# Kernel tuning notes

Hardware: AMD Instinct MI355X
Metric: run time of the kernel (lower is better)

Reference implementation:

```python
import jax, jax.numpy as jnp
import numpy as np

N_NODES = 100000
N_EDGES = 800000
HIDDEN = 128


def setup_inputs() -> dict:
    key = jax.random.key(0)
    k1, k2, k3, k4, k5, k6 = jax.random.split(key, 6)
    z = jax.random.normal(k1, (N_NODES, HIDDEN), dtype=jnp.float32)
    edge_index = jax.random.randint(k2, (2, N_EDGES), 0, N_NODES, dtype=jnp.int64)
    # nn.Linear params (torch default init scale ~ 1/sqrt(fan_in))
    s1 = 1.0 / np.sqrt(2 * HIDDEN)
    s2 = 1.0 / np.sqrt(HIDDEN)
    W1 = jax.random.uniform(k3, (2 * HIDDEN, HIDDEN), jnp.float32, -s1, s1)
    b1 = jax.random.uniform(k4, (HIDDEN,), jnp.float32, -s1, s1)
    W2 = jax.random.uniform(k5, (HIDDEN, 1), jnp.float32, -s2, s2)
    b2 = jax.random.uniform(k6, (1,), jnp.float32, -s2, s2)
    return {"z": z, "edge_index": edge_index, "W1": W1, "b1": b1, "W2": W2, "b2": b2}


def reference(z, edge_index, W1, b1, W2, b2):
    src, dst = edge_index[0], edge_index[1]
    # Gather endpoint features: [E, H] each. Avoid materializing the [E, 2H]
    # concat by splitting W1 into src/dst halves (same math as cat + matmul).
    W1_src, W1_dst = W1[:HIDDEN], W1[HIDDEN:]
    h = z[src] @ W1_src + z[dst] @ W1_dst + b1  # [E, H]
    h = jax.nn.relu(h)
    score = h @ W2 + b2  # [E, 1]
    return score
```

## Files before the change

### kernel.cpp

```cpp
#include <hip/hip_runtime.h>
#include <hip/hip_bf16.h>

#define N_NODES 100000
#define N_EDGES 800000
#define HIDDEN 128
#define N_TILES 1563
#define PC_GRID 512

typedef short frag_ab __attribute__((ext_vector_type(8)));
typedef float frag_cd __attribute__((ext_vector_type(4)));

__device__ inline unsigned short f2b(float f) {
    union { float f; unsigned u; } x; x.f = f;
    return (unsigned short)((x.u + 0x7fffu + ((x.u >> 16) & 1u)) >> 16);
}

__device__ inline unsigned pk2(float x, float y) {
    union { __hip_bfloat162 h; unsigned u; } c;
    c.h = __float22bfloat162_rn(make_float2(x, y));
    return c.u;
}

__global__ __launch_bounds__(256) void transpose_w1(
    const float* __restrict__ W1, unsigned short* __restrict__ Bt)
{
    const int t  = threadIdx.x;
    const int nc = blockIdx.x * 4 + (t >> 6);
    const int k2 = (t & 63) * 2;
    const int col  = nc & 127;
    const int roff = (nc >= 128) ? 128 : 0;
    float f0 = W1[(size_t)(roff + k2)     * HIDDEN + col];
    float f1 = W1[(size_t)(roff + k2 + 1) * HIDDEN + col];
    *(unsigned*)(Bt + (size_t)nc * HIDDEN + k2) = (unsigned)f2b(f0) | ((unsigned)f2b(f1) << 16);
}

#define AS_STRIDE 136
#define CS_STRIDE 264

__global__ __launch_bounds__(256) void precompute_uv_mfma(
    const float* __restrict__ z, const unsigned short* __restrict__ Bt,
    const float* __restrict__ b1, unsigned short* __restrict__ UV)
{
    __shared__ unsigned short smem[64 * CS_STRIDE];
    const int t = threadIdx.x;
    const int lane = t & 63;
    const int w = t >> 6;
    const int wn = w * 64;
    const int g  = lane >> 4;
    const int lc = lane & 15;

    frag_ab b[4][4];
    float bias[4];
    #pragma unroll
    for (int nt = 0; nt < 4; ++nt) {
        int nc = wn + nt * 16 + lc;
        bias[nt] = (nc < HIDDEN) ? b1[nc] : 0.f;
        const unsigned short* brow = Bt + (size_t)nc * HIDDEN;
        #pragma unroll
        for (int q = 0; q < 4; ++q)
            b[nt][q] = *(const frag_ab*)(brow + q * 32 + g * 8);
    }

    int tile = blockIdx.x;
    uint2 pf[8];
    #pragma unroll
    for (int i = 0; i < 8; ++i) {
        int f4 = i * 256 + t;
        int m = tile * 64 + (f4 >> 5);
        if (m >= N_NODES) m = N_NODES - 1;
        float4 v = ((const float4*)z)[(size_t)m * 32 + (f4 & 31)];
        pf[i].x = pk2(v.x, v.y);
        pf[i].y = pk2(v.z, v.w);
    }

    while (true) {
        #pragma unroll
        for (int i = 0; i < 8; ++i) {
            int f4 = i * 256 + t;
            *(uint2*)&smem[(f4 >> 5) * AS_STRIDE + (f4 & 31) * 4] = pf[i];
        }
        __syncthreads();

        const int next = tile + PC_GRID;
        const bool have_next = (next < N_TILES);
        if (have_next) {
            #pragma unroll
            for (int i = 0; i < 8; ++i) {
                int f4 = i * 256 + t;
                int m = next * 64 + (f4 >> 5);
                if (m >= N_NODES) m = N_NODES - 1;
                float4 v = ((const float4*)z)[(size_t)m * 32 + (f4 & 31)];
                pf[i].x = pk2(v.x, v.y);
                pf[i].y = pk2(v.z, v.w);
            }
        }

        frag_cd acc[4][4];
        #pragma unroll
        for (int mt = 0; mt < 4; ++mt)
            #pragma unroll
            for (int nt = 0; nt < 4; ++nt)
                acc[mt][nt] = (frag_cd){0.f, 0.f, 0.f, 0.f};
        #pragma unroll
        for (int q = 0; q < 4; ++q) {
            frag_ab a[4];
            #pragma unroll
            for (int mt = 0; mt < 4; ++mt)
                a[mt] = *(const frag_ab*)&smem[(mt * 16 + lc) * AS_STRIDE + q * 32 + g * 8];
            #pragma unroll
            for (int mt = 0; mt < 4; ++mt)
                #pragma unroll
                for (int nt = 0; nt < 4; ++nt)
                    acc[mt][nt] = __builtin_amdgcn_mfma_f32_16x16x32_bf16(
                        a[mt], b[nt][q], acc[mt][nt], 0, 0, 0);
        }
        __syncthreads();

        #pragma unroll
        for (int nt = 0; nt < 4; ++nt) {
            int nc = wn + nt * 16 + lc;
            #pragma unroll
            for (int mt = 0; mt < 4; ++mt)
                #pragma unroll
                for (int r = 0; r < 4; ++r)
                    smem[(mt * 16 + g * 4 + r) * CS_STRIDE + nc] =
                        f2b(acc[mt][nt][r] + bias[nt]);
        }
        __syncthreads();

        const int m0 = tile * 64;
        #pragma unroll
        for (int i = 0; i < 8; ++i) {
            int f = i * 256 + t;
            int m = f >> 5;
            int c16 = f & 31;
            if (m0 + m < N_NODES) {
                uint4 val = *(const uint4*)&smem[m * CS_STRIDE + c16 * 8];
                *(uint4*)&UV[(size_t)(m0 + m) * 256 + c16 * 8] = val;
            }
        }
        if (!have_next) break;
        __syncthreads();
        tile = next;
    }
}

__device__ inline float2 bf2(unsigned u) {
    union { unsigned i; float f; } lo, hi;
    lo.i = u << 16;
    hi.i = u & 0xffff0000u;
    return make_float2(lo.f, hi.f);
}

__device__ inline float2 rfma2(unsigned u, unsigned v, float2 w, float2 acc) {
    float2 uf = bf2(u), vf = bf2(v);
    float2 s = make_float2(uf.x + vf.x, uf.y + vf.y);
    s.x = fmaxf(s.x, 0.f); s.y = fmaxf(s.y, 0.f);
    acc.x = __builtin_fmaf(s.x, w.x, acc.x);
    acc.y = __builtin_fmaf(s.y, w.y, acc.y);
    return acc;
}

__global__ __launch_bounds__(256) void edge_score(
    const int* __restrict__ ei, const unsigned short* __restrict__ UV,
    const float* __restrict__ W2, const float* __restrict__ B2,
    float* __restrict__ out)
{
    const int t = threadIdx.x;
    const int g = t & 7;
    const int slot = t >> 3;
    const int e0 = blockIdx.x * 64 + slot;
    const int e1 = e0 + 32;

    const float4* W24 = (const float4*)W2;
    const float4 w0 = W24[g * 4 + 0];
    const float4 w1 = W24[g * 4 + 1];
    const float4 w2 = W24[g * 4 + 2];
    const float4 w3 = W24[g * 4 + 3];

    const int s0 = ei[e0];
    const int d0 = ei[N_EDGES + e0];
    const int s1 = ei[e1];
    const int d1 = ei[N_EDGES + e1];

    const uint4* u0p = (const uint4*)(UV + (size_t)s0 * 256) + g * 2;
    const uint4* v0p = (const uint4*)(UV + (size_t)d0 * 256 + 128) + g * 2;
    const uint4* u1p = (const uint4*)(UV + (size_t)s1 * 256) + g * 2;
    const uint4* v1p = (const uint4*)(UV + (size_t)d1 * 256 + 128) + g * 2;
    const uint4 ua0 = u0p[0], ub0 = u0p[1];
    const uint4 va0 = v0p[0], vb0 = v0p[1];
    const uint4 ua1 = u1p[0], ub1 = u1p[1];
    const uint4 va1 = v1p[0], vb1 = v1p[1];

    float2 A = make_float2(0.f, 0.f), B = make_float2(0.f, 0.f);
    A = rfma2(ua0.x, va0.x, make_float2(w0.x, w0.y), A);
    A = rfma2(ua0.y, va0.y, make_float2(w0.z, w0.w), A);
    A = rfma2(ua0.z, va0.z, make_float2(w1.x, w1.y), A);
    A = rfma2(ua0.w, va0.w, make_float2(w1.z, w1.w), A);
    A = rfma2(ub0.x, vb0.x, make_float2(w2.x, w2.y), A);
    A = rfma2(ub0.y, vb0.y, make_float2(w2.z, w2.w), A);
    A = rfma2(ub0.z, vb0.z, make_float2(w3.x, w3.y), A);
    A = rfma2(ub0.w, vb0.w, make_float2(w3.z, w3.w), A);

    B = rfma2(ua1.x, va1.x, make_float2(w0.x, w0.y), B);
    B = rfma2(ua1.y, va1.y, make_float2(w0.z, w0.w), B);
    B = rfma2(ua1.z, va1.z, make_float2(w1.x, w1.y), B);
    B = rfma2(ua1.w, va1.w, make_float2(w1.z, w1.w), B);
    B = rfma2(ub1.x, vb1.x, make_float2(w2.x, w2.y), B);
    B = rfma2(ub1.y, vb1.y, make_float2(w2.z, w2.w), B);
    B = rfma2(ub1.z, vb1.z, make_float2(w3.x, w3.y), B);
    B = rfma2(ub1.w, vb1.w, make_float2(w3.z, w3.w), B);

    float sa = A.x + A.y;
    float sb = B.x + B.y;
    sa += __shfl_xor(sa, 1, 8);
    sa += __shfl_xor(sa, 2, 8);
    sa += __shfl_xor(sa, 4, 8);
    sb += __shfl_xor(sb, 1, 8);
    sb += __shfl_xor(sb, 2, 8);
    sb += __shfl_xor(sb, 4, 8);

    if (g == 0) {
        float bb = B2[0];
        out[e0] = sa + bb;
        out[e1] = sb + bb;
    }
}

extern "C" void kernel_launch(void* const* d_in, const int* in_sizes, int n_in,
                              void* d_out, int out_size, void* d_ws, size_t ws_size,
                              hipStream_t stream) {
    const float* z  = (const float*)d_in[0];
    const int*   ei = (const int*)d_in[1];
    const float* W1 = (const float*)d_in[2];
    const float* b1 = (const float*)d_in[3];
    const float* W2 = (const float*)d_in[4];
    const float* b2 = (const float*)d_in[5];
    float* out = (float*)d_out;

    unsigned short* UV = (unsigned short*)d_ws;
    unsigned short* Bt = UV + (size_t)N_NODES * 256;

    transpose_w1<<<64, 256, 0, stream>>>(W1, Bt);
    precompute_uv_mfma<<<PC_GRID, 256, 0, stream>>>(z, Bt, b1, UV);
    edge_score<<<N_EDGES / 64, 256, 0, stream>>>(ei, UV, W2, b2, out);
}
```

Baseline: 162.7 us.

## Quantize per-node U/V projections to int8 with per-row scales

The precomputed per-node U/V projections are now quantized from bf16 to 8-bit values, each with a per-node, per-half absmax scale. The scale is found with a warp-shuffle max reduction over an fp32 staging buffer in shared memory. The edge kernel gathers half as many bytes per endpoint plus one scale each and dequantizes inline with FMAs before the ReLU and dot product. This targets the random-gather memory traffic that dominates edge scoring, in exchange for more ALU work, a larger shared-memory tile, and lower numerical precision that could exceed tolerance.

```diff
diff --git a/kernel.cpp b/kernel.cpp
--- a/kernel.cpp
+++ b/kernel.cpp
@@ -35,13 +35,14 @@
 }
 
 #define AS_STRIDE 136
-#define CS_STRIDE 264
 
 __global__ __launch_bounds__(256) void precompute_uv_mfma(
     const float* __restrict__ z, const unsigned short* __restrict__ Bt,
-    const float* __restrict__ b1, unsigned short* __restrict__ UV)
+    const float* __restrict__ b1, unsigned char* __restrict__ UVq,
+    float* __restrict__ scales)
 {
-    __shared__ unsigned short smem[64 * CS_STRIDE];
+    __shared__ float smemf[64 * 256];
+    unsigned short* smem = (unsigned short*)smemf;
     const int t = threadIdx.x;
     const int lane = t & 63;
     const int w = t >> 6;
@@ -122,49 +123,63 @@
             #pragma unroll
             for (int mt = 0; mt < 4; ++mt)
                 #pragma unroll
-                for (int r = 0; r < 4; ++r)
-                    smem[(mt * 16 + g * 4 + r) * CS_STRIDE + nc] =
-                        f2b(acc[mt][nt][r] + bias[nt]);
+                for (int r = 0; r < 4; ++r) {
+                    int row = mt * 16 + g * 4 + r;
+                    smemf[row * 256 + (nc ^ (g << 4))] = acc[mt][nt][r] + bias[nt];
+                }
         }
         __syncthreads();
 
         const int m0 = tile * 64;
         #pragma unroll
-        for (int i = 0; i < 8; ++i) {
-            int f = i * 256 + t;
-            int m = f >> 5;
-            int c16 = f & 31;
-            if (m0 + m < N_NODES) {
-                uint4 val = *(const uint4*)&smem[m * CS_STRIDE + c16 * 8];
-                *(uint4*)&UV[(size_t)(m0 + m) * 256 + c16 * 8] = val;
+        for (int it = 0; it < 16; ++it) {
+            const int row  = it * 4 + w;
+            const int node = m0 + row;
+            const int c    = (it & 3) << 4;
+            float4 x = *(const float4*)&smemf[row * 256 + ((lane * 4) ^ c)];
+            float mx = fmaxf(fmaxf(fabsf(x.x), fabsf(x.y)),
+                             fmaxf(fabsf(x.z), fabsf(x.w)));
+            #pragma unroll
+            for (int k = 1; k < 32; k <<= 1)
+                mx = fmaxf(mx, __shfl_xor(mx, k, 32));
+            mx = fmaxf(mx, 1e-12f);
+            const float ainv = 127.0f / mx;
+            unsigned q0 = (unsigned)__builtin_fmaf(x.x, ainv, 128.5f);
+            unsigned q1 = (unsigned)__builtin_fmaf(x.y, ainv, 128.5f);
+            unsigned q2 = (unsigned)__builtin_fmaf(x.z, ainv, 128.5f);
+            unsigned q3 = (unsigned)__builtin_fmaf(x.w, ainv, 128.5f);
+            unsigned pack = q0 | (q1 << 8) | (q2 << 16) | (q3 << 24);
+            if (node < N_NODES) {
+                *(unsigned*)&UVq[(size_t)node * 256 + lane * 4] = pack;
+                if ((lane & 31) == 0)
+                    scales[node * 2 + (lane >> 5)] = mx * (1.0f / 127.0f);
             }
         }
+
         if (!have_next) break;
         __syncthreads();
         tile = next;
     }
 }
 
-__device__ inline float2 bf2(unsigned u) {
-    union { unsigned i; float f; } lo, hi;
-    lo.i = u << 16;
-    hi.i = u & 0xffff0000u;
-    return make_float2(lo.f, hi.f);
-}
-
-__device__ inline float2 rfma2(unsigned u, unsigned v, float2 w, float2 acc) {
-    float2 uf = bf2(u), vf = bf2(v);
-    float2 s = make_float2(uf.x + vf.x, uf.y + vf.y);
-    s.x = fmaxf(s.x, 0.f); s.y = fmaxf(s.y, 0.f);
-    acc.x = __builtin_fmaf(s.x, w.x, acc.x);
-    acc.y = __builtin_fmaf(s.y, w.y, acc.y);
+__device__ inline float dq4(unsigned uq, unsigned vq, float aU, float aV,
+                            float k, float4 w, float acc) {
+    #pragma unroll
+    for (int b = 0; b < 4; ++b) {
+        float uf = (float)((uq >> (8 * b)) & 0xffu);
+        float vf = (float)((vq >> (8 * b)) & 0xffu);
+        float h  = __builtin_fmaf(aU, uf, __builtin_fmaf(aV, vf, k));
+        h = fmaxf(h, 0.f);
+        float wv = (b == 0) ? w.x : (b == 1) ? w.y : (b == 2) ? w.z : w.w;
+        acc = __builtin_fmaf(h, wv, acc);
+    }
     return acc;
 }
 
 __global__ __launch_bounds__(256) void edge_score(
-    const int* __restrict__ ei, const unsigned short* __restrict__ UV,
-    const float* __restrict__ W2, const float* __restrict__ B2,
-    float* __restrict__ out)
+    const int* __restrict__ ei, const unsigned char* __restrict__ UVq,
+    const float* __restrict__ scales, const float* __restrict__ W2,
+    const float* __restrict__ B2, float* __restrict__ out)
 {
     const int t = threadIdx.x;
     const int g = t & 7;
@@ -183,36 +198,31 @@
     const int s1 = ei[e1];
     const int d1 = ei[N_EDGES + e1];
 
-    const uint4* u0p = (const uint4*)(UV + (size_t)s0 * 256) + g * 2;
-    const uint4* v0p = (const uint4*)(UV + (size_t)d0 * 256 + 128) + g * 2;
-    const uint4* u1p = (const uint4*)(UV + (size_t)s1 * 256) + g * 2;
-    const uint4* v1p = (const uint4*)(UV + (size_t)d1 * 256 + 128) + g * 2;
-    const uint4 ua0 = u0p[0], ub0 = u0p[1];
-    const uint4 va0 = v0p[0], vb0 = v0p[1];
-    const uint4 ua1 = u1p[0], ub1 = u1p[1];
-    const uint4 va1 = v1p[0], vb1 = v1p[1];
-
-    float2 A = make_float2(0.f, 0.f), B = make_float2(0.f, 0.f);
-    A = rfma2(ua0.x, va0.x, make_float2(w0.x, w0.y), A);
-    A = rfma2(ua0.y, va0.y, make_float2(w0.z, w0.w), A);
-    A = rfma2(ua0.z, va0.z, make_float2(w1.x, w1.y), A);
-    A = rfma2(ua0.w, va0.w, make_float2(w1.z, w1.w), A);
-    A = rfma2(ub0.x, vb0.x, make_float2(w2.x, w2.y), A);
-    A = rfma2(ub0.y, vb0.y, make_float2(w2.z, w2.w), A);
-    A = rfma2(ub0.z, vb0.z, make_float2(w3.x, w3.y), A);
-    A = rfma2(ub0.w, vb0.w, make_float2(w3.z, w3.w), A);
-
-    B = rfma2(ua1.x, va1.x, make_float2(w0.x, w0.y), B);
-    B = rfma2(ua1.y, va1.y, make_float2(w0.z, w0.w), B);
-    B = rfma2(ua1.z, va1.z, make_float2(w1.x, w1.y), B);
-    B = rfma2(ua1.w, va1.w, make_float2(w1.z, w1.w), B);
-    B = rfma2(ub1.x, vb1.x, make_float2(w2.x, w2.y), B);
-    B = rfma2(ub1.y, vb1.y, make_float2(w2.z, w2.w), B);
-    B = rfma2(ub1.z, vb1.z, make_float2(w3.x, w3.y), B);
-    B = rfma2(ub1.w, vb1.w, make_float2(w3.z, w3.w), B);
-
-    float sa = A.x + A.y;
-    float sb = B.x + B.y;
+    const uint4 u0 = *(const uint4*)(UVq + (size_t)s0 * 256 + g * 16);
+    const uint4 v0 = *(const uint4*)(UVq + (size_t)d0 * 256 + 128 + g * 16);
+    const uint4 u1 = *(const uint4*)(UVq + (size_t)s1 * 256 + g * 16);
+    const uint4 v1 = *(const uint4*)(UVq + (size_t)d1 * 256 + 128 + g * 16);
+    const float aU0 = scales[s0 * 2];
+    const float aV0 = scales[d0 * 2 + 1];
+    const float aU1 = scales[s1 * 2];
+    const float aV1 = scales[d1 * 2 + 1];
+
+    const float k0 = -128.f * (aU0 + aV0);
+    const float k1 = -128.f * (aU1 + aV1);
+
+    float A = 0.f, B = 0.f;
+    A = dq4(u0.x, v0.x, aU0, aV0, k0, w0, A);
+    A = dq4(u0.y, v0.y, aU0, aV0, k0, w1, A);
+    A = dq4(u0.z, v0.z, aU0, aV0, k0, w2, A);
+    A = dq4(u0.w, v0.w, aU0, aV0, k0, w3, A);
+
+    B = dq4(u1.x, v1.x, aU1, aV1, k1, w0, B);
+    B = dq4(u1.y, v1.y, aU1, aV1, k1, w1, B);
+    B = dq4(u1.z, v1.z, aU1, aV1, k1, w2, B);
+    B = dq4(u1.w, v1.w, aU1, aV1, k1, w3, B);
+
+    float sa = A;
+    float sb = B;
     sa += __shfl_xor(sa, 1, 8);
     sa += __shfl_xor(sa, 2, 8);
     sa += __shfl_xor(sa, 4, 8);
@@ -238,10 +248,11 @@
     const float* b2 = (const float*)d_in[5];
     float* out = (float*)d_out;
 
-    unsigned short* UV = (unsigned short*)d_ws;
-    unsigned short* Bt = UV + (size_t)N_NODES * 256;
+    unsigned char* UVq = (unsigned char*)d_ws;
+    float* scales = (float*)(UVq + (size_t)N_NODES * 256);
+    unsigned short* Bt = (unsigned short*)(scales + 2 * N_NODES);
 
     transpose_w1<<<64, 256, 0, stream>>>(W1, Bt);
-    precompute_uv_mfma<<<PC_GRID, 256, 0, stream>>>(z, Bt, b1, UV);
-    edge_score<<<N_EDGES / 64, 256, 0, stream>>>(ei, UV, W2, b2, out);
-}
+    precompute_uv_mfma<<<PC_GRID, 256, 0, stream>>>(z, Bt, b1, UVq, scales);
+    edge_score<<<N_EDGES / 64, 256, 0, stream>>>(ei, UVq, scales, W2, b2, out);
+}
```

Result: faster. 147.4 us (-9.4%).
